# Optimization experiments

Measured on AMD Instinct MI355X. Metric: run time of the kernel, lower is better.

The kernel has to match this reference:

```python
import jax, jax.numpy as jnp
import numpy as np

N_NODES = 8192
N_EDGES = 131072
BATCH = 2
HID = 256      # hidden_dim
MSG = 256      # message_dim
EDIM = 64      # edge feature dim
MLP_H = 512    # message MLP hidden width
OUT = 128      # readout dim
N_ITERS = 3


def setup_inputs() -> dict:
    key = jax.random.key(0)
    ks = jax.random.split(key, 20)
    s = 0.05  # small init so iterated GRU stays well-conditioned
    inp = {
        "edge_feat": jax.random.normal(ks[0], (N_EDGES, BATCH, EDIM), jnp.float32),
        "W1": jax.random.normal(ks[1], (HID + HID + EDIM, MLP_H), jnp.float32) * s,
        "b1": jnp.zeros((MLP_H,), jnp.float32),
        "W2": jax.random.normal(ks[2], (MLP_H, MSG), jnp.float32) * s,
        "b2": jnp.zeros((MSG,), jnp.float32),
        "Wr": jax.random.normal(ks[3], (MSG, HID), jnp.float32) * s,
        "Ur": jax.random.normal(ks[4], (HID, HID), jnp.float32) * s,
        "br": jnp.zeros((HID,), jnp.float32),
        "Wz": jax.random.normal(ks[5], (MSG, HID), jnp.float32) * s,
        "Uz": jax.random.normal(ks[6], (HID, HID), jnp.float32) * s,
        "bz": jnp.zeros((HID,), jnp.float32),
        "Wh": jax.random.normal(ks[7], (MSG, HID), jnp.float32) * s,
        "Uh": jax.random.normal(ks[8], (HID, HID), jnp.float32) * s,
        "bh": jnp.zeros((HID,), jnp.float32),
        "Wo": jax.random.normal(ks[9], (HID, OUT), jnp.float32) * s,
        "bo": jnp.zeros((OUT,), jnp.float32),
        "edge_src": jax.random.randint(ks[10], (N_EDGES,), 0, N_NODES, jnp.int32),
        "edge_dst": jax.random.randint(ks[11], (N_EDGES,), 0, N_NODES, jnp.int32),
    }
    return inp


def reference(edge_feat, W1, b1, W2, b2, Wr, Ur, br, Wz, Uz, bz,
              Wh, Uh, bh, Wo, bo, edge_src, edge_dst):
    # reset_hidden_states: zeros for hidden and persistent message accumulator
    h = jnp.zeros((N_NODES, BATCH, HID), edge_feat.dtype)
    m = jnp.zeros((N_NODES, BATCH, MSG), edge_feat.dtype)

    for _ in range(N_ITERS):
        # gather endpoint hiddens: h_v = receiver (dst), h_w = sender (src)
        h_v = h[edge_dst]                       # [E, B, HID]
        h_w = h[edge_src]                       # [E, B, HID]
        x = jnp.concatenate([h_v, h_w, edge_feat], axis=-1)  # [E, B, 576]
        # per-edge message MLP
        msg = jax.nn.relu(x @ W1 + b1) @ W2 + b2              # [E, B, MSG]
        # scatter-sum into receiving nodes; accumulator persists across iters
        m = m + jax.ops.segment_sum(msg, edge_dst, num_segments=N_NODES)
        # GRU vertex update: h = GRU(m, h)
        r = jax.nn.sigmoid(m @ Wr + h @ Ur + br)
        z = jax.nn.sigmoid(m @ Wz + h @ Uz + bz)
        h_tilde = jnp.tanh(m @ Wh + (r * h) @ Uh + bh)
        h = (1.0 - z) * h + z * h_tilde

    # readout: sum node hiddens, then linear
    g = jnp.sum(h, axis=0)                      # [B, HID]
    return g @ Wo + bo                          # [B, OUT]
```

## Files before the change

### kernel.cpp

```cpp
#include <hip/hip_runtime.h>
#include <hip/hip_bf16.h>

#define E_EDGES 131072
#define NNODES  8192
#define NB      16384
#define HID     256
#define EDIM    64
#define MLPH    512
#define OUTD    128
#define NIT     3
#define RB      32

typedef short s16x4 __attribute__((ext_vector_type(4)));
typedef short s16x8 __attribute__((ext_vector_type(8)));
typedef float f32x4 __attribute__((ext_vector_type(4)));
typedef float f32x2 __attribute__((ext_vector_type(2)));
typedef unsigned int u32x4 __attribute__((ext_vector_type(4)));

__device__ __forceinline__ short f2bf(float f){
  unsigned int x = __builtin_bit_cast(unsigned int, f);
  x += 0x7fffu + ((x >> 16) & 1u);
  return (short)(x >> 16);
}
__device__ __forceinline__ float bf2f(short s){
  unsigned int x = ((unsigned int)(unsigned short)s) << 16;
  return __builtin_bit_cast(float, x);
}
__device__ __forceinline__ void gload_lds16(const void* g, void* l){
  __builtin_amdgcn_global_load_lds(
      (const __attribute__((address_space(1))) void*)g,
      (__attribute__((address_space(3))) void*)l, 16, 0, 0);
}
#define MFMA16(a,b,c) __builtin_amdgcn_mfma_f32_16x16x32_bf16((a),(b),(c),0,0,0)

#if defined(__has_builtin)
#if __has_builtin(__builtin_amdgcn_cvt_pk_f32_fp8) && __has_builtin(__builtin_amdgcn_cvt_pk_fp8_f32)
#define FP8_HW 1
#endif
#endif
#ifndef FP8_HW
#define FP8_HW 0
#endif

__device__ __forceinline__ unsigned char enc_fp8_sw(float f){
  unsigned int b = __builtin_bit_cast(unsigned int, f);
  unsigned int s = (b >> 24) & 0x80u;
  float a = fabsf(f);
  if (a >= 448.f) return (unsigned char)(s | 0x7e);
  if (a < 0.015625f){
    int q = (int)rintf(a * 512.f);
    return (unsigned char)(s | (unsigned int)q);
  }
  unsigned int e32  = (b >> 23) & 0xff;
  unsigned int mant = b & 0x7fffff;
  unsigned int rnd  = mant + 0x7ffff + ((mant >> 20) & 1);
  unsigned int e8   = e32 - 120 + (rnd >> 23);
  unsigned int m3   = (rnd >> 20) & 7;
  if (e8 >= 16) return (unsigned char)(s | 0x7e);
  return (unsigned char)(s | (e8 << 3) | m3);
}
__device__ __forceinline__ float dec_fp8_sw(unsigned int v){
  unsigned int s = (v >> 7) & 1, e = (v >> 3) & 15, m = v & 7;
  float r;
  if (e == 0) r = (float)m * 0.001953125f;
  else        r = __builtin_bit_cast(float, ((e + 120u) << 23) | (m << 20));
  return s ? -r : r;
}
__device__ __forceinline__ unsigned char enc_fp8(float f){
#if FP8_HW
  unsigned int pk = (unsigned int)__builtin_amdgcn_cvt_pk_fp8_f32(f, f, 0, false);
  return (unsigned char)(pk & 0xff);
#else
  return enc_fp8_sw(f);
#endif
}
__device__ __forceinline__ void dec_fp8x4(unsigned int ev, float& e0, float& e1,
                                          float& e2, float& e3){
#if FP8_HW
  f32x2 lo = __builtin_amdgcn_cvt_pk_f32_fp8((int)ev, false);
  f32x2 hi = __builtin_amdgcn_cvt_pk_f32_fp8((int)ev, true);
  e0 = lo[0]; e1 = lo[1]; e2 = hi[0]; e3 = hi[1];
#else
  e0 = dec_fp8_sw(ev & 0xff); e1 = dec_fp8_sw((ev >> 8) & 0xff);
  e2 = dec_fp8_sw((ev >> 16) & 0xff); e3 = dec_fp8_sw(ev >> 24);
#endif
}

__global__ __launch_bounds__(256, 3)
void e1_gemm(const float* __restrict__ ef, const short* __restrict__ BtE,
             unsigned char* __restrict__ E1, const float* __restrict__ b1,
             const int* __restrict__ ceid)
{
  __shared__ __align__(16) short As[128 * 64];
  __shared__ __align__(16) short Bs[128 * 64];
  __shared__ __align__(16) unsigned char Ts[128 * 128];

  const int t  = threadIdx.x;
  const int w  = t >> 6, l = t & 63;
  const int lr = l & 15, lg = l >> 4;
  const int wr = w >> 1, wc = w & 1;
  const int browbase = blockIdx.x * 128;
  const int srow = t >> 3;
  const int scol = (t & 7) * 8;

#pragma unroll
  for (int i = 0; i < 4; ++i){
    int R = browbase + srow + i * 32;
    int e = ceid[R >> 1];
    const float* ap = ef + ((size_t)e * 2 + (R & 1)) * EDIM + scol;
    f32x4 f0 = *(const f32x4*)ap;
    f32x4 f1 = *(const f32x4*)(ap + 4);
    s16x8 o;
    o[0]=f2bf(f0[0]); o[1]=f2bf(f0[1]); o[2]=f2bf(f0[2]); o[3]=f2bf(f0[3]);
    o[4]=f2bf(f1[0]); o[5]=f2bf(f1[1]); o[6]=f2bf(f1[2]); o[7]=f2bf(f1[3]);
    int row = srow + i * 32;
    *(s16x8*)(As + row * 64 + (scol ^ ((row & 7) << 3))) = o;
  }

  for (int pn = 0; pn < 4; ++pn){
#pragma unroll
    for (int i = 0; i < 4; ++i)
      gload_lds16(BtE + (size_t)(pn * 128 + srow + i * 32) * 64 + scol,
                  (char*)Bs + w * 1024 + i * 4096);
    __syncthreads();

    f32x4 acc[4][4];
#pragma unroll
    for (int mf = 0; mf < 4; ++mf)
#pragma unroll
      for (int e2 = 0; e2 < 4; ++e2) acc[mf][e2] = (f32x4){0.f,0.f,0.f,0.f};

#pragma unroll
    for (int kk = 0; kk < 2; ++kk){
      s16x8 a[4], b[4];
#pragma unroll
      for (int e2 = 0; e2 < 4; ++e2){
        int ar = wr*64 + e2*16 + lr;
        a[e2] = *(const s16x8*)(As + ar * 64 + ((kk*32 + lg*8) ^ ((ar & 7) << 3)));
      }
#pragma unroll
      for (int mf = 0; mf < 4; ++mf){
        int br = wc*64 + mf*16 + lr;
        b[mf] = *(const s16x8*)(Bs + br * 64 + ((kk*32 + lg*8) ^ ((br & 7) << 3)));
      }
#pragma unroll
      for (int mf = 0; mf < 4; ++mf)
#pragma unroll
        for (int e2 = 0; e2 < 4; ++e2)
          acc[mf][e2] = MFMA16(b[mf], a[e2], acc[mf][e2]);
    }

#pragma unroll
    for (int mf = 0; mf < 4; ++mf){
      int mloc = wc*64 + mf*16 + lg*4;
      f32x4 bv = *(const f32x4*)(b1 + pn*128 + mloc);
      int u = mloc >> 2;
      int usw_hi = (u >> 2), ulo = (u & 3) << 2;
#pragma unroll
      for (int e2 = 0; e2 < 4; ++e2){
        int erow = wr*64 + e2*16 + lr;
        unsigned int pk = (unsigned int)enc_fp8(acc[mf][e2][0] + bv[0])
                        | ((unsigned int)enc_fp8(acc[mf][e2][1] + bv[1]) << 8)
                        | ((unsigned int)enc_fp8(acc[mf][e2][2] + bv[2]) << 16)
                        | ((unsigned int)enc_fp8(acc[mf][e2][3] + bv[3]) << 24);
        *(unsigned int*)(Ts + erow * 128 + ((usw_hi ^ (erow & 7)) << 4) + ulo) = pk;
      }
    }
    __syncthreads();

    {
      int rr = t >> 1, hh = t & 1;
#pragma unroll
      for (int q = 0; q < 4; ++q){
        int u16 = q * 2 + hh;
        u32x4 v = *(const u32x4*)(Ts + rr * 128 + ((u16 ^ (rr & 7)) << 4));
        *(u32x4*)(E1 + (size_t)(browbase + rr) * 512 + pn * 128 + u16 * 16) = v;
      }
    }
  }
}

template<bool USE_P>
__global__ __launch_bounds__(256)
void edge_kernel(const short* __restrict__ P, const unsigned char* __restrict__ E1,
                 const int* __restrict__ csr_src, const int* __restrict__ row_start,
                 short* __restrict__ S)
{
  const int n = blockIdx.x;
  const int t = threadIdx.x;
  const int b = t >> 7;
  const int j = (t & 127) << 2;
  const int ps = row_start[n], pe = row_start[n + 1];

  float p10 = 0.f, p11 = 0.f, p12 = 0.f, p13 = 0.f;
  if (USE_P){
    s16x4 t1 = *(const s16x4*)(P + (size_t)(n * 2 + b) * 1024 + j);
    p10 = bf2f(t1[0]); p11 = bf2f(t1[1]); p12 = bf2f(t1[2]); p13 = bf2f(t1[3]);
  }
  float a0 = 0.f, a1 = 0.f, a2 = 0.f, a3 = 0.f;
  for (int p = ps; p < pe; ++p){
    unsigned int ev = *(const unsigned int*)(E1 + ((size_t)p * 2 + b) * 512 + j);
    float e0, e1, e2, e3;
    dec_fp8x4(ev, e0, e1, e2, e3);
    float x0 = p10 + e0, x1 = p11 + e1, x2 = p12 + e2, x3 = p13 + e3;
    if (USE_P){
      int src = csr_src[p];
      s16x4 v2 = *(const s16x4*)(P + (size_t)(src * 2 + b) * 1024 + 512 + j);
      x0 += bf2f(v2[0]); x1 += bf2f(v2[1]); x2 += bf2f(v2[2]); x3 += bf2f(v2[3]);
    }
    a0 += fmaxf(x0, 0.f); a1 += fmaxf(x1, 0.f);
    a2 += fmaxf(x2, 0.f); a3 += fmaxf(x3, 0.f);
  }
  s16x4 o; o[0] = f2bf(a0); o[1] = f2bf(a1); o[2] = f2bf(a2); o[3] = f2bf(a3);
  *(s16x4*)(S + (size_t)(n * 2 + b) * 512 + j) = o;
}

template<int PH>
__global__ __launch_bounds__(512, 4)
void node_update(const short* __restrict__ S, short* __restrict__ Pout,
                 float* __restrict__ m, float* __restrict__ h,
                 float* __restrict__ g,
                 const short* __restrict__ BtW2, const short* __restrict__ BtRZ,
                 const short* __restrict__ BtHW, const short* __restrict__ BtP,
                 const int* __restrict__ deg, const float* __restrict__ b2,
                 const float* __restrict__ br, const float* __restrict__ bz,
                 const float* __restrict__ bh)
{
  __shared__ __align__(16) char lds[69632];
  short* As = (short*)lds;
  short* Bs = (short*)(lds + 4096);
  short* Ms = (short*)(lds + 36864);
  short* Xs = (short*)(lds + 53248);
  float* Hf = (float*)lds;

  const int tid = threadIdx.x;
  const int w = tid >> 6, l = tid & 63;
  const int lr = l & 15, lg = l >> 4;
  const int wq = w >> 2, wc = w & 3;
  const int grow0 = blockIdx.x * RB;

  auto stageB = [&](const short* Bt, int K, int pcol0, int k0){
#pragma unroll
    for (int i = 0; i < 4; ++i){
      int u = i * 512 + tid;
      int row = u >> 3, uc = u & 7;
      const short* gp = Bt + (size_t)(pcol0 + row) * K + k0 + ((uc ^ (row & 7)) << 3);
      gload_lds16(gp, (char*)Bs + i * 8192 + w * 1024);
    }
  };
  auto stageA_S = [&](int k0){
    if (w < 4){
      int u = w * 64 + l;
      int row = u >> 3, uc = u & 7;
      const short* gp = S + (size_t)(grow0 + row) * 512 + k0 + ((uc ^ (row & 7)) << 3);
      gload_lds16(gp, (char*)As + w * 1024);
    }
  };
  auto rdA64 = [&](int row, int colel){ return row * 64 + (colel ^ ((row & 7) << 3)); };
  auto rd256 = [&](int row, int colel){ return row * 256 + (colel ^ ((row & 7) << 3)); };

  f32x4 hv[4], acc[4];
#pragma unroll
  for (int j = 0; j < 4; ++j)
#pragma unroll
    for (int r = 0; r < 4; ++r){
      int rl = wq*16 + lg*4 + r, colp = wc*64 + j*16 + lr;
      size_t gi = (size_t)(grow0 + rl) * 256 + colp;
      float base = (float)deg[(grow0 + rl) >> 1] * b2[colp];
      if (PH > 0){ base += m[gi]; hv[j][r] = h[gi]; }
      else hv[j][r] = 0.f;
      acc[j][r] = base;
    }
  if (PH > 0){
#pragma unroll
    for (int j = 0; j < 4; ++j)
#pragma unroll
      for (int r = 0; r < 4; ++r){
        int rl = wq*16 + lg*4 + r, colp = wc*64 + j*16 + lr;
        Xs[rd256(rl, colp)] = f2bf(hv[j][r]);
      }
  }

  for (int c = 0; c < 8; ++c){
    __syncthreads();
    stageA_S(c * 64);
    stageB(BtW2, 512, 0, c * 64);
    __syncthreads();
#pragma unroll
    for (int kk = 0; kk < 2; ++kk){
      s16x8 a0 = *(const s16x8*)(As + rdA64(wq*16 + lr, kk*32 + lg*8));
#pragma unroll
      for (int j = 0; j < 4; ++j){
        s16x8 bb = *(const s16x8*)(Bs + rdA64(wc*64 + j*16 + lr, kk*32 + lg*8));
        acc[j] = MFMA16(a0, bb, acc[j]);
      }
    }
  }
#pragma unroll
  for (int j = 0; j < 4; ++j)
#pragma unroll
    for (int r = 0; r < 4; ++r){
      int rl = wq*16 + lg*4 + r, colp = wc*64 + j*16 + lr;
      float v = acc[j][r];
      if (PH < 2) m[(size_t)(grow0 + rl) * 256 + colp] = v;
      Ms[rd256(rl, colp)] = f2bf(v);
    }

  const int NC = (PH > 0) ? 8 : 4;

  f32x4 Gr[4], Gz[4];
#pragma unroll
  for (int j = 0; j < 4; ++j){ Gr[j] = (f32x4){0.f,0.f,0.f,0.f}; Gz[j] = (f32x4){0.f,0.f,0.f,0.f}; }

  for (int c = 0; c < NC; ++c){
    __syncthreads();
    stageB(BtRZ, 512, 0, c * 64);
    __syncthreads();
    const short* Ab = (c < 4) ? Ms : Xs;
    int kb = (c & 3) * 64;
#pragma unroll
    for (int kk = 0; kk < 2; ++kk){
      s16x8 a0 = *(const s16x8*)(Ab + rd256(wq*16 + lr, kb + kk*32 + lg*8));
#pragma unroll
      for (int j = 0; j < 4; ++j){
        s16x8 bb = *(const s16x8*)(Bs + rdA64(wc*64 + j*16 + lr, kk*32 + lg*8));
        Gr[j] = MFMA16(a0, bb, Gr[j]);
      }
    }
  }
  for (int c = 0; c < NC; ++c){
    __syncthreads();
    stageB(BtRZ, 512, 256, c * 64);
    __syncthreads();
    const short* Ab = (c < 4) ? Ms : Xs;
    int kb = (c & 3) * 64;
#pragma unroll
    for (int kk = 0; kk < 2; ++kk){
      s16x8 a0 = *(const s16x8*)(Ab + rd256(wq*16 + lr, kb + kk*32 + lg*8));
#pragma unroll
      for (int j = 0; j < 4; ++j){
        s16x8 bb = *(const s16x8*)(Bs + rdA64(wc*64 + j*16 + lr, kk*32 + lg*8));
        Gz[j] = MFMA16(a0, bb, Gz[j]);
      }
    }
  }

  f32x4 zz[4];
#pragma unroll
  for (int j = 0; j < 4; ++j)
#pragma unroll
    for (int r = 0; r < 4; ++r){
      int colp = wc*64 + j*16 + lr;
      zz[j][r] = 1.f / (1.f + __expf(-(Gz[j][r] + bz[colp])));
    }
  if (PH > 0){
    __syncthreads();
#pragma unroll
    for (int j = 0; j < 4; ++j)
#pragma unroll
      for (int r = 0; r < 4; ++r){
        int rl = wq*16 + lg*4 + r, colp = wc*64 + j*16 + lr;
        float rr = 1.f / (1.f + __expf(-(Gr[j][r] + br[colp])));
        Xs[rd256(rl, colp)] = f2bf(rr * hv[j][r]);
      }
    __syncthreads();
  }

  f32x4 Gw[4];
#pragma unroll
  for (int j = 0; j < 4; ++j) Gw[j] = (f32x4){0.f,0.f,0.f,0.f};
  for (int c = 0; c < NC; ++c){
    __syncthreads();
    stageB(BtHW, 512, 0, c * 64);
    __syncthreads();
    const short* Ab = (c < 4) ? Ms : Xs;
    int kb = (c & 3) * 64;
#pragma unroll
    for (int kk = 0; kk < 2; ++kk){
      s16x8 a0 = *(const s16x8*)(Ab + rd256(wq*16 + lr, kb + kk*32 + lg*8));
#pragma unroll
      for (int j = 0; j < 4; ++j){
        s16x8 bb = *(const s16x8*)(Bs + rdA64(wc*64 + j*16 + lr, kk*32 + lg*8));
        Gw[j] = MFMA16(a0, bb, Gw[j]);
      }
    }
  }

  __syncthreads();
#pragma unroll
  for (int j = 0; j < 4; ++j)
#pragma unroll
    for (int r = 0; r < 4; ++r){
      int rl = wq*16 + lg*4 + r, colp = wc*64 + j*16 + lr;
      float ht = tanhf(Gw[j][r] + bh[colp]);
      float z  = zz[j][r];
      float hn = (1.f - z) * hv[j][r] + z * ht;
      if (PH < 2){
        h[(size_t)(grow0 + rl) * 256 + colp] = hn;
        Ms[rd256(rl, colp)] = f2bf(hn);
      } else {
        Hf[rl * 256 + colp] = hn;
      }
    }
  __syncthreads();

  if (PH < 2){
    for (int pn = 0; pn < 4; ++pn){
      f32x4 pa[4];
#pragma unroll
      for (int j = 0; j < 4; ++j) pa[j] = (f32x4){0.f,0.f,0.f,0.f};
      for (int c = 0; c < 4; ++c){
        __syncthreads();
        stageB(BtP, 256, pn * 256, c * 64);
        __syncthreads();
#pragma unroll
        for (int kk = 0; kk < 2; ++kk){
          s16x8 a0 = *(const s16x8*)(Ms + rd256(wq*16 + lr, c*64 + kk*32 + lg*8));
#pragma unroll
          for (int j = 0; j < 4; ++j){
            s16x8 bb = *(const s16x8*)(Bs + rdA64(wc*64 + j*16 + lr, kk*32 + lg*8));
            pa[j] = MFMA16(a0, bb, pa[j]);
          }
        }
      }
#pragma unroll
      for (int j = 0; j < 4; ++j)
#pragma unroll
        for (int r = 0; r < 4; ++r){
          int colp = wc*64 + j*16 + lr;
          Pout[(size_t)(grow0 + wq*16 + lg*4 + r) * 1024 + pn*256 + colp] = f2bf(pa[j][r]);
        }
    }
  } else {
    int col = tid & 255, pb = (tid >> 8) & 1;
    float s = 0.f;
#pragma unroll
    for (int rr = 0; rr < 16; ++rr)
      s += Hf[(2*rr + pb) * 256 + col];
    atomicAdd(&g[pb * 256 + col], s);
  }
}

__global__ void count_kernel(const int* __restrict__ edst, int* __restrict__ counts){
  int e = blockIdx.x * 256 + threadIdx.x;
  if (e < E_EDGES) atomicAdd(&counts[edst[e]], 1);
}
__global__ void scan_kernel(const int* __restrict__ counts, int* __restrict__ row_start,
                            int* __restrict__ cursor){
  __shared__ int sums[1024];
  int t = threadIdx.x;
  int base = t * 8;
  int loc[8]; int s = 0;
#pragma unroll
  for (int i = 0; i < 8; ++i){ loc[i] = s; s += counts[base + i]; }
  sums[t] = s;
  __syncthreads();
  for (int o = 1; o < 1024; o <<= 1){
    int v = sums[t];
    int u = (t >= o) ? sums[t - o] : 0;
    __syncthreads();
    sums[t] = v + u;
    __syncthreads();
  }
  int excl = (t == 0) ? 0 : sums[t - 1];
#pragma unroll
  for (int i = 0; i < 8; ++i){ int v = excl + loc[i]; row_start[base + i] = v; cursor[base + i] = v; }
  if (t == 1023) row_start[NNODES] = sums[1023];
}
__global__ void fill_kernel(const int* __restrict__ edst, const int* __restrict__ esrc,
                            int* __restrict__ cursor, int* __restrict__ csr_eid,
                            int* __restrict__ csr_src){
  int e = blockIdx.x * 256 + threadIdx.x;
  if (e < E_EDGES){
    int pos = atomicAdd(&cursor[edst[e]], 1);
    csr_eid[pos] = e;
    csr_src[pos] = esrc[e];
  }
}

__global__ void prep_weights(const float* __restrict__ W1, const float* __restrict__ W2,
                             const float* __restrict__ Wr, const float* __restrict__ Ur,
                             const float* __restrict__ Wz, const float* __restrict__ Uz,
                             const float* __restrict__ Wh, const float* __restrict__ Uh,
                             short* __restrict__ BtP, short* __restrict__ BtE,
                             short* __restrict__ BtW2, short* __restrict__ BtRZ,
                             short* __restrict__ BtHW)
{
  int id = blockIdx.x * 256 + threadIdx.x;
  if (id < 262144){
    int jj = id >> 8, k = id & 255;
    float v = (jj < 512) ? W1[(size_t)k * 512 + jj] : W1[(size_t)(256 + k) * 512 + (jj - 512)];
    BtP[id] = f2bf(v);
  } else if (id < 294912){
    int i2 = id - 262144; int jj = i2 >> 6, c = i2 & 63;
    BtE[jj * 64 + (c ^ ((jj & 7) << 3))] = f2bf(W1[(size_t)(512 + c) * 512 + jj]);
  } else if (id < 425984){
    int i2 = id - 294912; int n = i2 >> 9, k = i2 & 511;
    BtW2[i2] = f2bf(W2[(size_t)k * 256 + n]);
  } else if (id < 688128){
    int i2 = id - 425984; int col = i2 >> 9, k = i2 & 511;
    float v;
    if (col < 256) v = (k < 256) ? Wr[(size_t)k * 256 + col] : Ur[(size_t)(k - 256) * 256 + col];
    else { int c2 = col - 256; v = (k < 256) ? Wz[(size_t)k * 256 + c2] : Uz[(size_t)(k - 256) * 256 + c2]; }
    BtRZ[i2] = f2bf(v);
  } else if (id < 819200){
    int i2 = id - 688128; int col = i2 >> 9, k = i2 & 511;
    float v = (k < 256) ? Wh[(size_t)k * 256 + col] : Uh[(size_t)(k - 256) * 256 + col];
    BtHW[i2] = f2bf(v);
  }
}

__global__ __launch_bounds__(256)
void readout2(const float* __restrict__ g, const float* __restrict__ Wo,
              const float* __restrict__ bo, float* __restrict__ out){
  int t = threadIdx.x;
  int b = t >> 7, o = t & 127;
  float s = bo[o];
  for (int c = 0; c < 256; ++c) s += g[b * 256 + c] * Wo[c * 128 + o];
  out[b * 128 + o] = s;
}

extern "C" void kernel_launch(void* const* d_in, const int* in_sizes, int n_in,
                              void* d_out, int out_size, void* d_ws, size_t ws_size,
                              hipStream_t stream)
{
  const float* ef  = (const float*)d_in[0];
  const float* W1  = (const float*)d_in[1];
  const float* b1  = (const float*)d_in[2];
  const float* W2  = (const float*)d_in[3];
  const float* b2  = (const float*)d_in[4];
  const float* Wr  = (const float*)d_in[5];
  const float* Ur  = (const float*)d_in[6];
  const float* br  = (const float*)d_in[7];
  const float* Wz  = (const float*)d_in[8];
  const float* Uz  = (const float*)d_in[9];
  const float* bz  = (const float*)d_in[10];
  const float* Wh  = (const float*)d_in[11];
  const float* Uh  = (const float*)d_in[12];
  const float* bh  = (const float*)d_in[13];
  const float* Wo  = (const float*)d_in[14];
  const float* bo  = (const float*)d_in[15];
  const int* esrc  = (const int*)d_in[16];
  const int* edst  = (const int*)d_in[17];

  char* base = (char*)d_ws;
  size_t off = 0;
  auto alloc = [&](size_t bytes) -> char* {
    off = (off + 255) & ~(size_t)255;
    char* p = base + off;
    off += bytes;
    return p;
  };
  float* h    = (float*)alloc((size_t)NB * 256 * 4);
  float* m    = (float*)alloc((size_t)NB * 256 * 4);
  short* P    = (short*)alloc((size_t)NB * 1024 * 2);
  short* S    = (short*)alloc((size_t)NB * 512 * 2);
  unsigned char* E1 = (unsigned char*)alloc((size_t)E_EDGES * 2 * MLPH);
  short* BtP  = (short*)alloc(262144 * 2);
  short* BtE  = (short*)alloc(32768 * 2);
  short* BtW2 = (short*)alloc(131072 * 2);
  short* BtRZ = (short*)alloc(262144 * 2);
  short* BtHW = (short*)alloc(131072 * 2);
  int* counts = (int*)alloc(NNODES * 4);
  int* rs     = (int*)alloc((NNODES + 1) * 4);
  int* cursor = (int*)alloc(NNODES * 4);
  int* ceid   = (int*)alloc(E_EDGES * 4);
  int* csrc   = (int*)alloc(E_EDGES * 4);
  float* g    = (float*)alloc(512 * 4);

  dim3 blk(256);

  hipMemsetAsync(g,  0, 512 * 4, stream);
  hipMemsetAsync(counts, 0, NNODES * 4, stream);
  prep_weights<<<3200, blk, 0, stream>>>(W1, W2, Wr, Ur, Wz, Uz, Wh, Uh,
                                         BtP, BtE, BtW2, BtRZ, BtHW);
  count_kernel<<<512, blk, 0, stream>>>(edst, counts);
  scan_kernel<<<1, 1024, 0, stream>>>(counts, rs, cursor);
  fill_kernel<<<512, blk, 0, stream>>>(edst, esrc, cursor, ceid, csrc);

  e1_gemm<<<E_EDGES * 2 / 128, blk, 0, stream>>>(ef, BtE, E1, b1, ceid);

  edge_kernel<false><<<NNODES, blk, 0, stream>>>(P, E1, csrc, rs, S);
  node_update<0><<<NB / RB, dim3(512), 0, stream>>>(S, P, m, h, g,
      BtW2, BtRZ, BtHW, BtP, counts, b2, br, bz, bh);

  edge_kernel<true><<<NNODES, blk, 0, stream>>>(P, E1, csrc, rs, S);
  node_update<1><<<NB / RB, dim3(512), 0, stream>>>(S, P, m, h, g,
      BtW2, BtRZ, BtHW, BtP, counts, b2, br, bz, bh);

  edge_kernel<true><<<NNODES, blk, 0, stream>>>(P, E1, csrc, rs, S);
  node_update<2><<<NB / RB, dim3(512), 0, stream>>>(S, P, m, h, g,
      BtW2, BtRZ, BtHW, BtP, counts, b2, br, bz, bh);

  readout2<<<1, blk, 0, stream>>>(g, Wo, bo, (float*)d_out);
}
```

Measured before the change: 419.7 us.

## Double node_update row tile to 64 rows per block for weight reuse

```diff
diff --git a/kernel.cpp b/kernel.cpp
--- a/kernel.cpp
+++ b/kernel.cpp
@@ -9,7 +9,7 @@
 #define MLPH    512
 #define OUTD    128
 #define NIT     3
-#define RB      32
+#define RB      64
 
 typedef short s16x4 __attribute__((ext_vector_type(4)));
 typedef short s16x8 __attribute__((ext_vector_type(8)));
@@ -216,7 +216,7 @@
 }
 
 template<int PH>
-__global__ __launch_bounds__(512, 4)
+__global__ __launch_bounds__(512, 2)
 void node_update(const short* __restrict__ S, short* __restrict__ Pout,
                  float* __restrict__ m, float* __restrict__ h,
                  float* __restrict__ g,
@@ -226,17 +226,18 @@
                  const float* __restrict__ br, const float* __restrict__ bz,
                  const float* __restrict__ bh)
 {
-  __shared__ __align__(16) char lds[69632];
+  __shared__ __align__(16) char lds[106496];
   short* As = (short*)lds;
-  short* Bs = (short*)(lds + 4096);
-  short* Ms = (short*)(lds + 36864);
-  short* Xs = (short*)(lds + 53248);
+  short* Bs = (short*)(lds + 8192);
+  short* Ms = (short*)(lds + 40960);
+  short* Xs = (short*)(lds + 73728);
   float* Hf = (float*)lds;
 
   const int tid = threadIdx.x;
   const int w = tid >> 6, l = tid & 63;
   const int lr = l & 15, lg = l >> 4;
   const int wq = w >> 2, wc = w & 3;
+  const int rb = wq * 32;
   const int grow0 = blockIdx.x * RB;
 
   auto stageB = [&](const short* Bt, int K, int pcol0, int k0){
@@ -249,36 +250,37 @@
     }
   };
   auto stageA_S = [&](int k0){
-    if (w < 4){
-      int u = w * 64 + l;
-      int row = u >> 3, uc = u & 7;
-      const short* gp = S + (size_t)(grow0 + row) * 512 + k0 + ((uc ^ (row & 7)) << 3);
-      gload_lds16(gp, (char*)As + w * 1024);
-    }
+    int row = tid >> 3, uc = tid & 7;
+    const short* gp = S + (size_t)(grow0 + row) * 512 + k0 + ((uc ^ (row & 7)) << 3);
+    gload_lds16(gp, (char*)As + w * 1024);
   };
   auto rdA64 = [&](int row, int colel){ return row * 64 + (colel ^ ((row & 7) << 3)); };
   auto rd256 = [&](int row, int colel){ return row * 256 + (colel ^ ((row & 7) << 3)); };
 
-  f32x4 hv[4], acc[4];
-#pragma unroll
-  for (int j = 0; j < 4; ++j)
-#pragma unroll
-    for (int r = 0; r < 4; ++r){
-      int rl = wq*16 + lg*4 + r, colp = wc*64 + j*16 + lr;
-      size_t gi = (size_t)(grow0 + rl) * 256 + colp;
-      float base = (float)deg[(grow0 + rl) >> 1] * b2[colp];
-      if (PH > 0){ base += m[gi]; hv[j][r] = h[gi]; }
-      else hv[j][r] = 0.f;
-      acc[j][r] = base;
-    }
+  f32x4 hv[2][4], acc[2][4];
+#pragma unroll
+  for (int i = 0; i < 2; ++i)
+#pragma unroll
+    for (int j = 0; j < 4; ++j)
+#pragma unroll
+      for (int r = 0; r < 4; ++r){
+        int rl = rb + i*16 + lg*4 + r, colp = wc*64 + j*16 + lr;
+        size_t gi = (size_t)(grow0 + rl) * 256 + colp;
+        float base = (float)deg[(grow0 + rl) >> 1] * b2[colp];
+        if (PH > 0){ base += m[gi]; hv[i][j][r] = h[gi]; }
+        else hv[i][j][r] = 0.f;
+        acc[i][j][r] = base;
+      }
   if (PH > 0){
 #pragma unroll
-    for (int j = 0; j < 4; ++j)
-#pragma unroll
-      for (int r = 0; r < 4; ++r){
-        int rl = wq*16 + lg*4 + r, colp = wc*64 + j*16 + lr;
-        Xs[rd256(rl, colp)] = f2bf(hv[j][r]);
-      }
+    for (int i = 0; i < 2; ++i)
+#pragma unroll
+      for (int j = 0; j < 4; ++j)
+#pragma unroll
+        for (int r = 0; r < 4; ++r){
+          int rl = rb + i*16 + lg*4 + r, colp = wc*64 + j*16 + lr;
+          Xs[rd256(rl, colp)] = f2bf(hv[i][j][r]);
+        }
   }
 
   for (int c = 0; c < 8; ++c){
@@ -288,29 +290,35 @@
     __syncthreads();
 #pragma unroll
     for (int kk = 0; kk < 2; ++kk){
-      s16x8 a0 = *(const s16x8*)(As + rdA64(wq*16 + lr, kk*32 + lg*8));
+      s16x8 a0 = *(const s16x8*)(As + rdA64(rb + lr,      kk*32 + lg*8));
+      s16x8 a1 = *(const s16x8*)(As + rdA64(rb + 16 + lr, kk*32 + lg*8));
 #pragma unroll
       for (int j = 0; j < 4; ++j){
         s16x8 bb = *(const s16x8*)(Bs + rdA64(wc*64 + j*16 + lr, kk*32 + lg*8));
-        acc[j] = MFMA16(a0, bb, acc[j]);
-      }
-    }
-  }
-#pragma unroll
-  for (int j = 0; j < 4; ++j)
-#pragma unroll
-    for (int r = 0; r < 4; ++r){
-      int rl = wq*16 + lg*4 + r, colp = wc*64 + j*16 + lr;
-      float v = acc[j][r];
-      if (PH < 2) m[(size_t)(grow0 + rl) * 256 + colp] = v;
-      Ms[rd256(rl, colp)] = f2bf(v);
-    }
+        acc[0][j] = MFMA16(a0, bb, acc[0][j]);
+        acc[1][j] = MFMA16(a1, bb, acc[1][j]);
+      }
+    }
+  }
+#pragma unroll
+  for (int i = 0; i < 2; ++i)
+#pragma unroll
+    for (int j = 0; j < 4; ++j)
+#pragma unroll
+      for (int r = 0; r < 4; ++r){
+        int rl = rb + i*16 + lg*4 + r, colp = wc*64 + j*16 + lr;
+        float v = acc[i][j][r];
+        if (PH < 2) m[(size_t)(grow0 + rl) * 256 + colp] = v;
+        Ms[rd256(rl, colp)] = f2bf(v);
+      }
 
   const int NC = (PH > 0) ? 8 : 4;
 
-  f32x4 Gr[4], Gz[4];
-#pragma unroll
-  for (int j = 0; j < 4; ++j){ Gr[j] = (f32x4){0.f,0.f,0.f,0.f}; Gz[j] = (f32x4){0.f,0.f,0.f,0.f}; }
+  f32x4 Gr[2][4], Gz[2][4];
+#pragma unroll
+  for (int i = 0; i < 2; ++i)
+#pragma unroll
+    for (int j = 0; j < 4; ++j){ Gr[i][j] = (f32x4){0.f,0.f,0.f,0.f}; Gz[i][j] = (f32x4){0.f,0.f,0.f,0.f}; }
 
   for (int c = 0; c < NC; ++c){
     __syncthreads();
@@ -320,11 +328,13 @@
     int kb = (c & 3) * 64;
 #pragma unroll
     for (int kk = 0; kk < 2; ++kk){
-      s16x8 a0 = *(const s16x8*)(Ab + rd256(wq*16 + lr, kb + kk*32 + lg*8));
+      s16x8 a0 = *(const s16x8*)(Ab + rd256(rb + lr,      kb + kk*32 + lg*8));
+      s16x8 a1 = *(const s16x8*)(Ab + rd256(rb + 16 + lr, kb + kk*32 + lg*8));
 #pragma unroll
       for (int j = 0; j < 4; ++j){
         s16x8 bb = *(const s16x8*)(Bs + rdA64(wc*64 + j*16 + lr, kk*32 + lg*8));
-        Gr[j] = MFMA16(a0, bb, Gr[j]);
+        Gr[0][j] = MFMA16(a0, bb, Gr[0][j]);
+        Gr[1][j] = MFMA16(a1, bb, Gr[1][j]);
       }
     }
   }
@@ -336,39 +346,47 @@
     int kb = (c & 3) * 64;
 #pragma unroll
     for (int kk = 0; kk < 2; ++kk){
-      s16x8 a0 = *(const s16x8*)(Ab + rd256(wq*16 + lr, kb + kk*32 + lg*8));
+      s16x8 a0 = *(const s16x8*)(Ab + rd256(rb + lr,      kb + kk*32 + lg*8));
+      s16x8 a1 = *(const s16x8*)(Ab + rd256(rb + 16 + lr, kb + kk*32 + lg*8));
 #pragma unroll
       for (int j = 0; j < 4; ++j){
         s16x8 bb = *(const s16x8*)(Bs + rdA64(wc*64 + j*16 + lr, kk*32 + lg*8));
-        Gz[j] = MFMA16(a0, bb, Gz[j]);
-      }
-    }
-  }
-
-  f32x4 zz[4];
-#pragma unroll
-  for (int j = 0; j < 4; ++j)
-#pragma unroll
-    for (int r = 0; r < 4; ++r){
-      int colp = wc*64 + j*16 + lr;
-      zz[j][r] = 1.f / (1.f + __expf(-(Gz[j][r] + bz[colp])));
-    }
+        Gz[0][j] = MFMA16(a0, bb, Gz[0][j]);
+        Gz[1][j] = MFMA16(a1, bb, Gz[1][j]);
+      }
+    }
+  }
+
+  f32x4 zz[2][4];
+#pragma unroll
+  for (int i = 0; i < 2; ++i)
+#pragma unroll
+    for (int j = 0; j < 4; ++j)
+#pragma unroll
+      for (int r = 0; r < 4; ++r){
+        int colp = wc*64 + j*16 + lr;
+        zz[i][j][r] = 1.f / (1.f + __expf(-(Gz[i][j][r] + bz[colp])));
+      }
   if (PH > 0){
     __syncthreads();
 #pragma unroll
-    for (int j = 0; j < 4; ++j)
-#pragma unroll
-      for (int r = 0; r < 4; ++r){
-        int rl = wq*16 + lg*4 + r, colp = wc*64 + j*16 + lr;
-        float rr = 1.f / (1.f + __expf(-(Gr[j][r] + br[colp])));
-        Xs[rd256(rl, colp)] = f2bf(rr * hv[j][r]);
-      }
-    __syncthreads();
-  }
-
-  f32x4 Gw[4];
-#pragma unroll
-  for (int j = 0; j < 4; ++j) Gw[j] = (f32x4){0.f,0.f,0.f,0.f};
+    for (int i = 0; i < 2; ++i)
+#pragma unroll
+      for (int j = 0; j < 4; ++j)
+#pragma unroll
+        for (int r = 0; r < 4; ++r){
+          int rl = rb + i*16 + lg*4 + r, colp = wc*64 + j*16 + lr;
+          float rr = 1.f / (1.f + __expf(-(Gr[i][j][r] + br[colp])));
+          Xs[rd256(rl, colp)] = f2bf(rr * hv[i][j][r]);
+        }
+    __syncthreads();
+  }
+
+  f32x4 Gw[2][4];
+#pragma unroll
+  for (int i = 0; i < 2; ++i)
+#pragma unroll
+    for (int j = 0; j < 4; ++j) Gw[i][j] = (f32x4){0.f,0.f,0.f,0.f};
   for (int c = 0; c < NC; ++c){
     __syncthreads();
     stageB(BtHW, 512, 0, c * 64);
@@ -377,49 +395,55 @@
     int kb = (c & 3) * 64;
 #pragma unroll
     for (int kk = 0; kk < 2; ++kk){
-      s16x8 a0 = *(const s16x8*)(Ab + rd256(wq*16 + lr, kb + kk*32 + lg*8));
+      s16x8 a0 = *(const s16x8*)(Ab + rd256(rb + lr,      kb + kk*32 + lg*8));
+      s16x8 a1 = *(const s16x8*)(Ab + rd256(rb + 16 + lr, kb + kk*32 + lg*8));
 #pragma unroll
       for (int j = 0; j < 4; ++j){
         s16x8 bb = *(const s16x8*)(Bs + rdA64(wc*64 + j*16 + lr, kk*32 + lg*8));
-        Gw[j] = MFMA16(a0, bb, Gw[j]);
+        Gw[0][j] = MFMA16(a0, bb, Gw[0][j]);
+        Gw[1][j] = MFMA16(a1, bb, Gw[1][j]);
       }
     }
   }
 
   __syncthreads();
 #pragma unroll
-  for (int j = 0; j < 4; ++j)
-#pragma unroll
-    for (int r = 0; r < 4; ++r){
-      int rl = wq*16 + lg*4 + r, colp = wc*64 + j*16 + lr;
-      float ht = tanhf(Gw[j][r] + bh[colp]);
-      float z  = zz[j][r];
-      float hn = (1.f - z) * hv[j][r] + z * ht;
-      if (PH < 2){
-        h[(size_t)(grow0 + rl) * 256 + colp] = hn;
-        Ms[rd256(rl, colp)] = f2bf(hn);
-      } else {
-        Hf[rl * 256 + colp] = hn;
-      }
-    }
+  for (int i = 0; i < 2; ++i)
+#pragma unroll
+    for (int j = 0; j < 4; ++j)
+#pragma unroll
+      for (int r = 0; r < 4; ++r){
+        int rl = rb + i*16 + lg*4 + r, colp = wc*64 + j*16 + lr;
+        float ht = tanhf(Gw[i][j][r] + bh[colp]);
+        float z  = zz[i][j][r];
+        float hn = (1.f - z) * hv[i][j][r] + z * ht;
+        if (PH < 2){
+          h[(size_t)(grow0 + rl) * 256 + colp] = hn;
+          Ms[rd256(rl, colp)] = f2bf(hn);
+        } else {
+          Hf[rl * 256 + colp] = hn;
+        }
+      }
   __syncthreads();
 
   if (PH < 2){
     for (int pn = 0; pn < 4; ++pn){
-      f32x4 pa[4];
-#pragma unroll
-      for (int j = 0; j < 4; ++j) pa[j] = (f32x4){0.f,0.f,0.f,0.f};
+      f32x4 pa0[4], pa1[4];
+#pragma unroll
+      for (int j = 0; j < 4; ++j){ pa0[j] = (f32x4){0.f,0.f,0.f,0.f}; pa1[j] = (f32x4){0.f,0.f,0.f,0.f}; }
       for (int c = 0; c < 4; ++c){
         __syncthreads();
         stageB(BtP, 256, pn * 256, c * 64);
         __syncthreads();
 #pragma unroll
         for (int kk = 0; kk < 2; ++kk){
-          s16x8 a0 = *(const s16x8*)(Ms + rd256(wq*16 + lr, c*64 + kk*32 + lg*8));
+          s16x8 a0 = *(const s16x8*)(Ms + rd256(rb + lr,      c*64 + kk*32 + lg*8));
+          s16x8 a1 = *(const s16x8*)(Ms + rd256(rb + 16 + lr, c*64 + kk*32 + lg*8));
 #pragma unroll
           for (int j = 0; j < 4; ++j){
             s16x8 bb = *(const s16x8*)(Bs + rdA64(wc*64 + j*16 + lr, kk*32 + lg*8));
-            pa[j] = MFMA16(a0, bb, pa[j]);
+            pa0[j] = MFMA16(a0, bb, pa0[j]);
+            pa1[j] = MFMA16(a1, bb, pa1[j]);
           }
         }
       }
@@ -428,14 +452,15 @@
 #pragma unroll
         for (int r = 0; r < 4; ++r){
           int colp = wc*64 + j*16 + lr;
-          Pout[(size_t)(grow0 + wq*16 + lg*4 + r) * 1024 + pn*256 + colp] = f2bf(pa[j][r]);
+          Pout[(size_t)(grow0 + rb + lg*4 + r)      * 1024 + pn*256 + colp] = f2bf(pa0[j][r]);
+          Pout[(size_t)(grow0 + rb + 16 + lg*4 + r) * 1024 + pn*256 + colp] = f2bf(pa1[j][r]);
         }
     }
   } else {
     int col = tid & 255, pb = (tid >> 8) & 1;
     float s = 0.f;
 #pragma unroll
-    for (int rr = 0; rr < 16; ++rr)
+    for (int rr = 0; rr < 32; ++rr)
       s += Hf[(2*rr + pb) * 256 + col];
     atomicAdd(&g[pb * 256 + col], s);
   }
```

Measured after the change: 438.8 us. +4.6%, slower.
